# Kernel tuning notes

Measured on AMD Instinct MI355X. Metric: run time of the kernel, lower is better.

## Reference

```python
import jax, jax.numpy as jnp
import numpy as np

N = 50000
E = 800000
D_IN = 384
D_H = 128
D_MLP = 128
K = 16


def layer_norm(x, g, b, eps=1e-5):
    m = x.mean(-1, keepdims=True)
    v = ((x - m) ** 2).mean(-1, keepdims=True)
    return (x - m) / jnp.sqrt(v + eps) * g + b


def setup_inputs() -> dict:
    key = jax.random.key(0)
    ks = jax.random.split(key, 16)
    s = lambda d: 1.0 / np.sqrt(d)
    return {
        "x": jax.random.normal(ks[0], (N, D_IN), jnp.float32),
        "edge_index": jax.random.randint(ks[1], (2, E), 0, N, jnp.int64),
        # GCNConv 1
        "W1": jax.random.normal(ks[2], (D_IN, D_H), jnp.float32) * s(D_IN),
        "b1": jnp.zeros((D_H,), jnp.float32),
        "g1": jnp.ones((D_H,), jnp.float32),
        "be1": jnp.zeros((D_H,), jnp.float32),
        # GCNConv 2
        "W2": jax.random.normal(ks[3], (D_H, D_H), jnp.float32) * s(D_H),
        "b2": jnp.zeros((D_H,), jnp.float32),
        "g2": jnp.ones((D_H,), jnp.float32),
        "be2": jnp.zeros((D_H,), jnp.float32),
        # residual projection (input_dim != conv_hidden)
        "rW": jax.random.normal(ks[4], (D_IN, D_H), jnp.float32) * s(D_IN),
        "rb": jnp.zeros((D_H,), jnp.float32),
        "rg": jnp.ones((D_H,), jnp.float32),
        "rbe": jnp.zeros((D_H,), jnp.float32),
        # MLP head
        "mW1": jax.random.normal(ks[5], (D_H, D_MLP), jnp.float32) * s(D_H),
        "mb1": jnp.zeros((D_MLP,), jnp.float32),
        "mg": jnp.ones((D_MLP,), jnp.float32),
        "mbe": jnp.zeros((D_MLP,), jnp.float32),
        "mW2": jax.random.normal(ks[6], (D_MLP, K), jnp.float32) * s(D_MLP),
        "mb2": jnp.zeros((K,), jnp.float32),
    }


def reference(x, edge_index, W1, b1, g1, be1, W2, b2, g2, be2,
              rW, rb, rg, rbe, mW1, mb1, mg, mbe, mW2, mb2):
    n = x.shape[0]
    loops = jnp.arange(n, dtype=edge_index.dtype)
    src = jnp.concatenate([edge_index[0], loops])  # [E+N]
    dst = jnp.concatenate([edge_index[1], loops])
    # symmetric GCN normalization with self-loops
    deg = jax.ops.segment_sum(jnp.ones_like(src, x.dtype), dst, num_segments=n)
    dinv = jnp.where(deg > 0, jax.lax.rsqrt(deg), 0.0)
    norm = dinv[src] * dinv[dst]  # [E+N]

    def gcn_conv(h, W, b):
        hw = h @ W  # [N, D_H]
        msg = hw[src] * norm[:, None]  # gather + scale, [E+N, D_H]
        return jax.ops.segment_sum(msg, dst, num_segments=n) + b

    # layer 1 with projected residual
    h = jax.nn.elu(layer_norm(gcn_conv(x, W1, b1), g1, be1))
    h = h + layer_norm(x @ rW + rb, rg, rbe)
    # layer 2 with identity residual
    h = jax.nn.elu(layer_norm(gcn_conv(h, W2, b2), g2, be2)) + h
    # MLP head (dropout inactive in eval) + softmax over clusters
    z = jax.nn.elu(layer_norm(h @ mW1 + mb1, mg, mbe))
    H = z @ mW2 + mb2
    return jax.nn.softmax(H, axis=1)
```

## Files before the change

kernel.cpp:

```cpp
#include <hip/hip_runtime.h>

#define DH 128

typedef __attribute__((ext_vector_type(8))) short short8;
typedef __attribute__((ext_vector_type(4))) float f32x4;

__device__ __forceinline__ float wave_sum(float v) {
    #pragma unroll
    for (int o = 32; o > 0; o >>= 1) v += __shfl_xor(v, o, 64);
    return v;
}

__device__ __forceinline__ void ln_pair(float v0, float v1, float& o0, float& o1) {
    float m = wave_sum(v0 + v1) * (1.f / 128.f);
    float d0 = v0 - m, d1 = v1 - m;
    float var = wave_sum(d0 * d0 + d1 * d1) * (1.f / 128.f);
    float inv = rsqrtf(var + 1e-5f);
    o0 = d0 * inv; o1 = d1 * inv;
}

__device__ __forceinline__ float elu(float x) { return x > 0.f ? x : expm1f(x); }

__device__ __forceinline__ unsigned short f2bf(float f) {
    unsigned u = __float_as_uint(f);
    u += 0x7fffu + ((u >> 16) & 1u);
    return (unsigned short)(u >> 16);
}
__device__ __forceinline__ float bfl(unsigned u) { return __uint_as_float(u << 16); }
__device__ __forceinline__ float bfh(unsigned u) { return __uint_as_float(u & 0xffff0000u); }
__device__ __forceinline__ unsigned pack_bf2(float a, float b) {
    return (unsigned)f2bf(a) | ((unsigned)f2bf(b) << 16);
}
__device__ __forceinline__ short8 cvt8(float4 v0, float4 v1) {
    short8 o;
    o[0] = (short)f2bf(v0.x); o[1] = (short)f2bf(v0.y);
    o[2] = (short)f2bf(v0.z); o[3] = (short)f2bf(v0.w);
    o[4] = (short)f2bf(v1.x); o[5] = (short)f2bf(v1.y);
    o[6] = (short)f2bf(v1.z); o[7] = (short)f2bf(v1.w);
    return o;
}

__device__ __forceinline__ int xcd_work(int bid, int nwg) {
    int qc = nwg >> 3, rc = nwg & 7;
    int xcd = bid & 7, ix = bid >> 3;
    return (xcd < rc ? xcd * (qc + 1) : rc * (qc + 1) + (xcd - rc) * qc) + ix;
}

__device__ __forceinline__ void gload_lds16(const unsigned short* gp, unsigned short* lp) {
    __builtin_amdgcn_global_load_lds(
        (const __attribute__((address_space(1))) void*)gp,
        (__attribute__((address_space(3))) void*)lp, 16, 0, 0);
}

__global__ __launch_bounds__(256) void conv_x_k(const float* __restrict__ x,
                                                unsigned short* __restrict__ xb,
                                                long long n8)
{
    long long i = (long long)blockIdx.x * 256 + threadIdx.x;
    long long stride = (long long)gridDim.x * 256;
    for (; i < n8; i += stride) {
        float4 v0 = *(const float4*)(x + i * 8);
        float4 v1 = *(const float4*)(x + i * 8 + 4);
        *(short8*)(xb + i * 8) = cvt8(v0, v1);
    }
}

__global__ void deg_count_k(const int* __restrict__ dst, int* __restrict__ deg, int E) {
    int e = blockIdx.x * 256 + threadIdx.x;
    if (e < E) atomicAdd(&deg[dst[e]], 1);
}

__global__ __launch_bounds__(1024) void scan_part_k(const int* __restrict__ deg,
                                                    int* __restrict__ rowptr,
                                                    int* __restrict__ bsum,
                                                    float* __restrict__ dinv, int n)
{
    __shared__ int wsum[16];
    const int tid = threadIdx.x, lane = tid & 63, wid = tid >> 6;
    int i = blockIdx.x * 1024 + tid;
    int v = (i < n) ? deg[i] : 0;
    if (i < n) dinv[i] = rsqrtf((float)(v + 1));
    int s = v;
    #pragma unroll
    for (int o = 1; o < 64; o <<= 1) {
        int t = __shfl_up(s, o, 64);
        if (lane >= o) s += t;
    }
    if (lane == 63) wsum[wid] = s;
    __syncthreads();
    if (tid < 16) {
        int ws = wsum[tid];
        #pragma unroll
        for (int o = 1; o < 16; o <<= 1) {
            int t = __shfl_up(ws, o, 64);
            if (tid >= o) ws += t;
        }
        wsum[tid] = ws;
    }
    __syncthreads();
    int excl = (wid ? wsum[wid - 1] : 0) + s - v;
    if (i < n) rowptr[i] = excl;
    if (tid == 0) bsum[blockIdx.x] = wsum[15];
}

__global__ void scan_top_k(int* __restrict__ bsum, int* __restrict__ rowptr_n, int nb) {
    int lane = threadIdx.x;
    int carry = 0;
    for (int base = 0; base < nb; base += 64) {
        int i = base + lane;
        int v = (i < nb) ? bsum[i] : 0;
        int s = v;
        #pragma unroll
        for (int o = 1; o < 64; o <<= 1) {
            int t = __shfl_up(s, o, 64);
            if (lane >= o) s += t;
        }
        if (i < nb) bsum[i] = carry + s - v;
        carry += __shfl(s, 63, 64);
    }
    if (lane == 0) *rowptr_n = carry;
}

__global__ void scan_add_k(const int* __restrict__ bsum, int* __restrict__ rowptr,
                           int* __restrict__ cursor, int n)
{
    int i = blockIdx.x * 256 + threadIdx.x;
    if (i < n) {
        int v = rowptr[i] + bsum[i >> 10];
        rowptr[i] = v;
        cursor[i] = v;
    }
}

__global__ __launch_bounds__(256) void fill_xcd_k(
    const int* __restrict__ src, const int* __restrict__ dst,
    const float* __restrict__ dinv, int* __restrict__ cursor,
    int2* __restrict__ csr, int E, int n)
{
    const int g   = blockIdx.x & 7;
    const int j   = blockIdx.x >> 3;
    const int bpg = gridDim.x >> 3;
    const int per = (n + 7) >> 3;
    const int lo = g * per;
    const int hi = min(n, lo + per);
    for (int e = j * 256 + threadIdx.x; e < E; e += bpg * 256) {
        int d = dst[e];
        if (d >= lo && d < hi) {
            int s = src[e];
            float w = dinv[s] * dinv[d];
            int p = atomicAdd(&cursor[d], 1);
            csr[p] = make_int2(s, __float_as_int(w));
        }
    }
}

__global__ void repack_zero_k(const float* __restrict__ W1, const float* __restrict__ rW,
                              const float* __restrict__ W2, const float* __restrict__ mW1,
                              unsigned short* __restrict__ Wp, int* __restrict__ deg, int n)
{
    int idx = blockIdx.x * 256 + threadIdx.x;
    if (idx < n) deg[idx] = 0;
    if (idx >= 131072) return;
    const float* W; int base;
    if (idx < 49152)       { W = W1;  base = 0; }
    else if (idx < 98304)  { W = rW;  base = 49152; }
    else if (idx < 114688) { W = W2;  base = 98304; }
    else                   { W = mW1; base = 114688; }
    int l = idx - base;
    int kb = l >> 12, rem = l & 4095;
    int nn = rem >> 5, ki = rem & 31;
    Wp[idx] = f2bf(W[(kb * 32 + ki) * DH + nn]);
}

__global__ __launch_bounds__(256, 3) void gemm1_k(
    const unsigned short* __restrict__ xb,
    const unsigned short* __restrict__ Bp1, const unsigned short* __restrict__ Bp2,
    const float* __restrict__ bb,
    unsigned short* __restrict__ outa, unsigned short* __restrict__ outb, int n)
{
    constexpr int NT = 6;
    __shared__ __align__(16) unsigned short smem[24576];
    unsigned short* smB = smem + 16384;

    const int tid = threadIdx.x;
    const int wid = tid >> 6, lane = tid & 63;
    const int m16 = lane & 15, q = lane >> 4;

    const int work = xcd_work(blockIdx.x, gridDim.x);
    const int rblk = work >> 2;
    const int var  = work & 3;
    const int mat = var >> 1;
    const int c0  = (var & 1) * 64;
    const unsigned short* Bp = mat ? Bp2 : Bp1;
    unsigned short* outp = mat ? outb : outa;
    const float* bias = mat ? bb : nullptr;
    const long long rowbase = (long long)rblk * 128;

    const unsigned short* gA[4];
    int ldsA[4];
    #pragma unroll
    for (int i = 0; i < 4; ++i) {
        int j = wid * 4 + i;
        int r = j * 8 + (lane >> 3);
        int c = lane & 7;
        long long gr = rowbase + r; if (gr > (long long)n - 1) gr = n - 1;
        gA[i] = xb + gr * 384 + ((c ^ (r & 7)) * 8);
        ldsA[i] = j * 512;
    }
    const unsigned short* gB[2];
    int ldsB[2];
    #pragma unroll
    for (int i = 0; i < 2; ++i) {
        int j2 = wid * 2 + i;
        int cl = j2 * 8 + (lane >> 3);
        int c = lane & 7;
        int cp = c ^ (cl & 7);
        gB[i] = Bp + (cp >> 2) * 4096 + (c0 + cl) * 32 + (cp & 3) * 8;
        ldsB[i] = j2 * 512;
    }

    auto issueT = [&](int t, int buf) {
        #pragma unroll
        for (int i = 0; i < 4; ++i)
            gload_lds16(gA[i] + t * 64, smem + buf * 8192 + ldsA[i]);
        #pragma unroll
        for (int i = 0; i < 2; ++i)
            gload_lds16(gB[i] + t * 8192, smB + buf * 4096 + ldsB[i]);
    };

    f32x4 acc[2][4];
    const f32x4 zero = {0.f, 0.f, 0.f, 0.f};
    #pragma unroll
    for (int mi = 0; mi < 2; ++mi)
        #pragma unroll
        for (int nj = 0; nj < 4; ++nj) acc[mi][nj] = zero;

    const int arow = wid * 32 + m16;
    const int s8a = m16 & 7;

    issueT(0, 0);
    __syncthreads();

    #pragma unroll
    for (int t = 0; t < NT; ++t) {
        const int buf = t & 1;
        if (t + 1 < NT) issueT(t + 1, buf ^ 1);
        const unsigned short* a0 = smem + buf * 8192;
        const unsigned short* b0 = smB + buf * 4096;
        short8 af[2][2], bf[2][4];
        #pragma unroll
        for (int ks = 0; ks < 2; ++ks) {
            int co = ((ks * 4 + q) ^ s8a) * 8;
            af[ks][0] = *(const short8*)(a0 + arow * 64 + co);
            af[ks][1] = *(const short8*)(a0 + (arow + 16) * 64 + co);
            #pragma unroll
            for (int nj = 0; nj < 4; ++nj)
                bf[ks][nj] = *(const short8*)(b0 + (nj * 16 + m16) * 64 + co);
        }
        #pragma unroll
        for (int ks = 0; ks < 2; ++ks)
            #pragma unroll
            for (int nj = 0; nj < 4; ++nj) {
                acc[0][nj] = __builtin_amdgcn_mfma_f32_16x16x32_bf16(af[ks][0], bf[ks][nj], acc[0][nj], 0, 0, 0);
                acc[1][nj] = __builtin_amdgcn_mfma_f32_16x16x32_bf16(af[ks][1], bf[ks][nj], acc[1][nj], 0, 0, 0);
            }
        __syncthreads();
    }

    #pragma unroll
    for (int nj = 0; nj < 4; ++nj) {
        int cl = nj * 16 + m16;
        float bv = bias ? bias[c0 + cl] : 0.f;
        #pragma unroll
        for (int mi = 0; mi < 2; ++mi)
            #pragma unroll
            for (int r = 0; r < 4; ++r)
                smem[(wid * 32 + mi * 16 + q * 4 + r) * 72 + cl] = f2bf(acc[mi][nj][r] + bv);
    }
    __syncthreads();
    #pragma unroll
    for (int h = 0; h < 4; ++h) {
        int idx = tid + h * 256;
        int row = idx >> 3, c8 = idx & 7;
        long long grow = rowbase + row;
        if (grow < n)
            *(short8*)(outp + grow * DH + c0 + c8 * 8) = *(const short8*)(smem + row * 72 + c8 * 8);
    }
}

__global__ __launch_bounds__(256, 3) void gemm_k128(
    const unsigned short* __restrict__ A,
    const unsigned short* __restrict__ Bp, const float* __restrict__ bias,
    unsigned short* __restrict__ outp, int n)
{
    __shared__ __align__(16) unsigned short smem[24576];
    unsigned short* smB = smem + 16384;

    const int tid = threadIdx.x;
    const int wid = tid >> 6, lane = tid & 63;
    const int m16 = lane & 15, q = lane >> 4;

    const int work = xcd_work(blockIdx.x, gridDim.x);
    const int rblk = work >> 1;
    const int c0 = (work & 1) * 64;
    const long long rowbase = (long long)rblk * 128;

    #pragma unroll
    for (int r = 0; r < 8; ++r) {
        int j = r * 256 + tid;
        int row = j >> 4, c16 = j & 15;
        long long grow = rowbase + row; if (grow > (long long)n - 1) grow = n - 1;
        *(short8*)(smem + row * 128 + ((c16 ^ (row & 15)) * 8)) =
            *(const short8*)(A + grow * 128 + c16 * 8);
    }
    #pragma unroll
    for (int r = 0; r < 4; ++r) {
        int j = r * 256 + tid;
        int kb = j >> 8, rem = j & 255;
        int cl = rem >> 2, qq = rem & 3;
        *(short8*)(smB + kb * 2048 + qq * 512 + cl * 8) =
            *(const short8*)(Bp + kb * 4096 + c0 * 32 + rem * 8);
    }
    __syncthreads();

    f32x4 acc[2][4];
    const f32x4 zero = {0.f, 0.f, 0.f, 0.f};
    #pragma unroll
    for (int mi = 0; mi < 2; ++mi)
        #pragma unroll
        for (int nj = 0; nj < 4; ++nj) acc[mi][nj] = zero;

    const int frow = wid * 32 + m16;
    #pragma unroll
    for (int kb = 0; kb < 4; ++kb) {
        short8 af0 = *(const short8*)(smem + frow * 128 + (((kb * 4 + q) ^ m16) * 8));
        short8 af1 = *(const short8*)(smem + (frow + 16) * 128 + (((kb * 4 + q) ^ m16) * 8));
        #pragma unroll
        for (int nj = 0; nj < 4; ++nj) {
            short8 bf = *(const short8*)(smB + kb * 2048 + q * 512 + (nj * 16 + m16) * 8);
            acc[0][nj] = __builtin_amdgcn_mfma_f32_16x16x32_bf16(af0, bf, acc[0][nj], 0, 0, 0);
            acc[1][nj] = __builtin_amdgcn_mfma_f32_16x16x32_bf16(af1, bf, acc[1][nj], 0, 0, 0);
        }
    }

    __syncthreads();
    #pragma unroll
    for (int nj = 0; nj < 4; ++nj) {
        int cl = nj * 16 + m16;
        float bv = bias ? bias[c0 + cl] : 0.f;
        #pragma unroll
        for (int mi = 0; mi < 2; ++mi)
            #pragma unroll
            for (int r = 0; r < 4; ++r)
                smem[(wid * 32 + mi * 16 + q * 4 + r) * 72 + cl] = f2bf(acc[mi][nj][r] + bv);
    }
    __syncthreads();
    #pragma unroll
    for (int h = 0; h < 4; ++h) {
        int idx = tid + h * 256;
        int row = idx >> 3, c8 = idx & 7;
        long long grow = rowbase + row;
        if (grow < n)
            *(short8*)(outp + grow * DH + c0 + c8 * 8) = *(const short8*)(smem + row * 72 + c8 * 8);
    }
}

__device__ __forceinline__ void gather_row(
    const unsigned* __restrict__ hw, const int2* __restrict__ csr,
    int beg, int end, int lane, float& o0, float& o1)
{
    beg = __builtin_amdgcn_readfirstlane(beg);
    end = __builtin_amdgcn_readfirstlane(end);
    float a0 = 0.f, a1 = 0.f, b0 = 0.f, b1 = 0.f;
    float c0 = 0.f, c1 = 0.f, d0 = 0.f, d1 = 0.f;
    int p = beg;
    for (; p + 15 < end; p += 16) {
        int2 e[16];
        #pragma unroll
        for (int i = 0; i < 16; ++i) e[i] = csr[p + i];
        unsigned u[16];
        #pragma unroll
        for (int i = 0; i < 16; ++i) u[i] = hw[(long long)e[i].x * 64 + lane];
        #pragma unroll
        for (int i = 0; i < 16; ++i) {
            float w = __int_as_float(e[i].y);
            float lo = bfl(u[i]), hi = bfh(u[i]);
            if ((i & 3) == 0)      { a0 = fmaf(w, lo, a0); a1 = fmaf(w, hi, a1); }
            else if ((i & 3) == 1) { b0 = fmaf(w, lo, b0); b1 = fmaf(w, hi, b1); }
            else if ((i & 3) == 2) { c0 = fmaf(w, lo, c0); c1 = fmaf(w, hi, c1); }
            else                   { d0 = fmaf(w, lo, d0); d1 = fmaf(w, hi, d1); }
        }
    }
    for (; p + 3 < end; p += 4) {
        int2 e0 = csr[p], e1 = csr[p + 1], e2 = csr[p + 2], e3 = csr[p + 3];
        unsigned u0 = hw[(long long)e0.x * 64 + lane];
        unsigned u1 = hw[(long long)e1.x * 64 + lane];
        unsigned u2 = hw[(long long)e2.x * 64 + lane];
        unsigned u3 = hw[(long long)e3.x * 64 + lane];
        float w0 = __int_as_float(e0.y), w1 = __int_as_float(e1.y);
        float w2 = __int_as_float(e2.y), w3 = __int_as_float(e3.y);
        a0 = fmaf(w0, bfl(u0), a0);  a1 = fmaf(w0, bfh(u0), a1);
        b0 = fmaf(w1, bfl(u1), b0);  b1 = fmaf(w1, bfh(u1), b1);
        c0 = fmaf(w2, bfl(u2), c0);  c1 = fmaf(w2, bfh(u2), c1);
        d0 = fmaf(w3, bfl(u3), d0);  d1 = fmaf(w3, bfh(u3), d1);
    }
    for (; p < end; ++p) {
        int2 e0 = csr[p];
        unsigned u0 = hw[(long long)e0.x * 64 + lane];
        float w0 = __int_as_float(e0.y);
        a0 = fmaf(w0, bfl(u0), a0);
        a1 = fmaf(w0, bfh(u0), a1);
    }
    o0 = (a0 + b0) + (c0 + d0);
    o1 = (a1 + b1) + (c1 + d1);
}

__global__ __launch_bounds__(256) void gfuse1_k(
    const unsigned* __restrict__ hw, const unsigned* __restrict__ proj,
    const int* __restrict__ rowptr, const int2* __restrict__ csr,
    const float* __restrict__ dinv,
    const float* __restrict__ b1, const float* __restrict__ g1, const float* __restrict__ be1,
    const float* __restrict__ rg, const float* __restrict__ rbe,
    unsigned* __restrict__ hout, int n)
{
    int row = blockIdx.x * 4 + (threadIdx.x >> 6);
    if (row >= n) return;
    int lane = threadIdx.x & 63;
    float a0, a1;
    gather_row(hw, csr, rowptr[row], rowptr[row + 1], lane, a0, a1);
    long long off = (long long)row * 64;
    float di = dinv[row], sl = di * di;
    unsigned us = hw[off + lane];
    float2 bv  = *(const float2*)(b1 + 2 * lane);
    float2 gv  = *(const float2*)(g1 + 2 * lane);
    float2 bev = *(const float2*)(be1 + 2 * lane);
    float2 rgv = *(const float2*)(rg + 2 * lane);
    float2 rbv = *(const float2*)(rbe + 2 * lane);
    float v0 = a0 + sl * bfl(us) + bv.x;
    float v1 = a1 + sl * bfh(us) + bv.y;
    float o0, o1; ln_pair(v0, v1, o0, o1);
    float t0 = elu(o0 * gv.x + bev.x);
    float t1 = elu(o1 * gv.y + bev.y);
    unsigned up = proj[off + lane];
    float q0, q1; ln_pair(bfl(up), bfh(up), q0, q1);
    hout[off + lane] = pack_bf2(t0 + q0 * rgv.x + rbv.x, t1 + q1 * rgv.y + rbv.y);
}

__global__ __launch_bounds__(256) void gfuse2_k(
    const unsigned* __restrict__ hw, const unsigned* __restrict__ hprev,
    const int* __restrict__ rowptr, const int2* __restrict__ csr,
    const float* __restrict__ dinv,
    const float* __restrict__ b2, const float* __restrict__ g2, const float* __restrict__ be2,
    unsigned* __restrict__ h2, int n)
{
    int row = blockIdx.x * 4 + (threadIdx.x >> 6);
    if (row >= n) return;
    int lane = threadIdx.x & 63;
    float a0, a1;
    gather_row(hw, csr, rowptr[row], rowptr[row + 1], lane, a0, a1);
    long long off = (long long)row * 64;
    float di = dinv[row], sl = di * di;
    unsigned us = hw[off + lane];
    float2 bv  = *(const float2*)(b2 + 2 * lane);
    float2 gv  = *(const float2*)(g2 + 2 * lane);
    float2 bev = *(const float2*)(be2 + 2 * lane);
    float v0 = a0 + sl * bfl(us) + bv.x;
    float v1 = a1 + sl * bfh(us) + bv.y;
    float o0, o1; ln_pair(v0, v1, o0, o1);
    float t0 = elu(o0 * gv.x + bev.x);
    float t1 = elu(o1 * gv.y + bev.y);
    unsigned uh = hprev[off + lane];
    h2[off + lane] = pack_bf2(t0 + bfl(uh), t1 + bfh(uh));
}

__global__ __launch_bounds__(256) void head_k(
    const unsigned* __restrict__ zraw, const float* __restrict__ g, const float* __restrict__ be,
    const float* __restrict__ mW2, const float* __restrict__ mb2,
    float* __restrict__ out, int n)
{
    int row = blockIdx.x * 4 + (threadIdx.x >> 6);
    if (row >= n) return;
    int lane = threadIdx.x & 63;
    unsigned u = zraw[(long long)row * 64 + lane];
    float o0, o1; ln_pair(bfl(u), bfh(u), o0, o1);
    float2 gv  = *(const float2*)(g + 2 * lane);
    float2 bev = *(const float2*)(be + 2 * lane);
    float z0 = elu(o0 * gv.x + bev.x);
    float z1 = elu(o1 * gv.y + bev.y);
    int k = lane & 15, seg = lane >> 4;
    float acc = 0.f;
    #pragma unroll
    for (int t = 0; t < 16; ++t) {
        int srcl = seg * 16 + t;
        float zz0 = __shfl(z0, srcl, 64);
        float zz1 = __shfl(z1, srcl, 64);
        int c = seg * 32 + 2 * t;
        acc = fmaf(zz0, mW2[c * 16 + k], acc);
        acc = fmaf(zz1, mW2[(c + 1) * 16 + k], acc);
    }
    acc += __shfl_xor(acc, 32, 64);
    acc += __shfl_xor(acc, 16, 64);
    float hk = acc + mb2[k];
    float mx = hk;
    #pragma unroll
    for (int o = 8; o > 0; o >>= 1) mx = fmaxf(mx, __shfl_xor(mx, o, 64));
    float e = expf(hk - mx);
    float s = e;
    #pragma unroll
    for (int o = 8; o > 0; o >>= 1) s += __shfl_xor(s, o, 64);
    if (lane < 16) out[(long long)row * 16 + k] = e / s;
}

static inline size_t align16(size_t x) { return (x + 15) & ~(size_t)15; }

extern "C" void kernel_launch(void* const* d_in, const int* in_sizes, int n_in,
                              void* d_out, int out_size, void* d_ws, size_t ws_size,
                              hipStream_t stream)
{
    const float* x   = (const float*)d_in[0];
    const int*   ei  = (const int*)d_in[1];
    const float* W1  = (const float*)d_in[2];
    const float* b1  = (const float*)d_in[3];
    const float* g1  = (const float*)d_in[4];
    const float* be1 = (const float*)d_in[5];
    const float* W2  = (const float*)d_in[6];
    const float* b2  = (const float*)d_in[7];
    const float* g2  = (const float*)d_in[8];
    const float* be2 = (const float*)d_in[9];
    const float* rW  = (const float*)d_in[10];
    const float* rb  = (const float*)d_in[11];
    const float* rg  = (const float*)d_in[12];
    const float* rbe = (const float*)d_in[13];
    const float* mW1 = (const float*)d_in[14];
    const float* mb1 = (const float*)d_in[15];
    const float* mg  = (const float*)d_in[16];
    const float* mbe = (const float*)d_in[17];
    const float* mW2 = (const float*)d_in[18];
    const float* mb2 = (const float*)d_in[19];
    float* out = (float*)d_out;

    const int n = in_sizes[0] / 384;
    const int E = in_sizes[1] / 2;
    const int* src = ei;
    const int* dst = ei + E;

    char* w = (char*)d_ws;
    int* deg     = (int*)w;   w += align16((size_t)n * 4);
    int* rowptr  = (int*)w;   w += align16((size_t)(n + 1) * 4);
    int* cursor  = (int*)w;   w += align16((size_t)n * 4);
    float* dinv  = (float*)w; w += align16((size_t)n * 4);
    int* bsum    = (int*)w;   w += align16((size_t)1024 * 4);
    int2* csr    = (int2*)w;  w += align16((size_t)E * 8);
    unsigned short* xb   = (unsigned short*)w; w += align16((size_t)n * 384 * 2);
    unsigned short* hw1  = (unsigned short*)w; w += align16((size_t)n * DH * 2);
    unsigned short* proj = (unsigned short*)w; w += align16((size_t)n * DH * 2);
    unsigned short* hbuf = (unsigned short*)w; w += align16((size_t)n * DH * 2);
    unsigned short* Wp   = (unsigned short*)w; w += align16((size_t)131072 * 2);
    unsigned short* Wp1 = Wp;
    unsigned short* Wpr = Wp + 49152;
    unsigned short* Wp2 = Wp + 98304;
    unsigned short* WpM = Wp + 114688;
    unsigned short* hw2  = hw1;
    unsigned short* h2   = proj;
    unsigned short* zraw = hbuf;

    int gE = (E + 255) / 256;
    int gN = (n + 255) / 256;
    int nb = (n + 1023) / 1024;
    int rblks = (n + 127) / 128;
    int gRow4 = (n + 3) / 4;

    conv_x_k<<<2048, 256, 0, stream>>>(x, xb, (long long)n * 48);
    repack_zero_k<<<512, 256, 0, stream>>>(W1, rW, W2, mW1, Wp, deg, n);

    deg_count_k<<<gE, 256, 0, stream>>>(dst, deg, E);
    scan_part_k<<<nb, 1024, 0, stream>>>(deg, rowptr, bsum, dinv, n);
    scan_top_k<<<1, 64, 0, stream>>>(bsum, rowptr + n, nb);
    scan_add_k<<<gN, 256, 0, stream>>>(bsum, rowptr, cursor, n);
    fill_xcd_k<<<1024, 256, 0, stream>>>(src, dst, dinv, cursor, csr, E, n);

    gemm1_k<<<rblks * 4, 256, 0, stream>>>(xb, Wp1, Wpr, rb, hw1, proj, n);
    gfuse1_k<<<gRow4, 256, 0, stream>>>((unsigned*)hw1, (unsigned*)proj, rowptr, csr, dinv,
                                        b1, g1, be1, rg, rbe, (unsigned*)hbuf, n);

    gemm_k128<<<rblks * 2, 256, 0, stream>>>(hbuf, Wp2, nullptr, hw2, n);
    gfuse2_k<<<gRow4, 256, 0, stream>>>((unsigned*)hw2, (unsigned*)hbuf, rowptr, csr, dinv,
                                        b2, g2, be2, (unsigned*)h2, n);

    gemm_k128<<<rblks * 2, 256, 0, stream>>>(h2, WpM, mb1, zraw, n);
    head_k<<<gRow4, 256, 0, stream>>>((unsigned*)zraw, mg, mbe, mW2, mb2, out, n);
}
```

Before: 402.3 us.

## Fuse fp32-to-bf16 input conversion into first GEMM by loading fp32 tiles to LDS

```diff
diff --git a/kernel.cpp b/kernel.cpp
--- a/kernel.cpp
+++ b/kernel.cpp
@@ -46,23 +46,10 @@
     return (xcd < rc ? xcd * (qc + 1) : rc * (qc + 1) + (xcd - rc) * qc) + ix;
 }
 
-__device__ __forceinline__ void gload_lds16(const unsigned short* gp, unsigned short* lp) {
+__device__ __forceinline__ void gload_lds16(const void* gp, void* lp) {
     __builtin_amdgcn_global_load_lds(
         (const __attribute__((address_space(1))) void*)gp,
         (__attribute__((address_space(3))) void*)lp, 16, 0, 0);
-}
-
-__global__ __launch_bounds__(256) void conv_x_k(const float* __restrict__ x,
-                                                unsigned short* __restrict__ xb,
-                                                long long n8)
-{
-    long long i = (long long)blockIdx.x * 256 + threadIdx.x;
-    long long stride = (long long)gridDim.x * 256;
-    for (; i < n8; i += stride) {
-        float4 v0 = *(const float4*)(x + i * 8);
-        float4 v1 = *(const float4*)(x + i * 8 + 4);
-        *(short8*)(xb + i * 8) = cvt8(v0, v1);
-    }
 }
 
 __global__ void deg_count_k(const int* __restrict__ dst, int* __restrict__ deg, int E) {
@@ -172,15 +159,16 @@
     Wp[idx] = f2bf(W[(kb * 32 + ki) * DH + nn]);
 }
 
-__global__ __launch_bounds__(256, 3) void gemm1_k(
-    const unsigned short* __restrict__ xb,
+__global__ __launch_bounds__(256, 2) void gemm1_k(
+    const float* __restrict__ x,
     const unsigned short* __restrict__ Bp1, const unsigned short* __restrict__ Bp2,
     const float* __restrict__ bb,
     unsigned short* __restrict__ outa, unsigned short* __restrict__ outb, int n)
 {
     constexpr int NT = 6;
-    __shared__ __align__(16) unsigned short smem[24576];
-    unsigned short* smB = smem + 16384;
+    __shared__ __align__(16) unsigned char smraw[81920];
+    float* smA = (float*)smraw;
+    unsigned short* smB = (unsigned short*)(smraw + 65536);
 
     const int tid = threadIdx.x;
     const int wid = tid >> 6, lane = tid & 63;
@@ -196,16 +184,16 @@
     const float* bias = mat ? bb : nullptr;
     const long long rowbase = (long long)rblk * 128;
 
-    const unsigned short* gA[4];
-    int ldsA[4];
-    #pragma unroll
-    for (int i = 0; i < 4; ++i) {
-        int j = wid * 4 + i;
-        int r = j * 8 + (lane >> 3);
-        int c = lane & 7;
+    const float* gA[8];
+    int ldsA[8];
+    #pragma unroll
+    for (int i = 0; i < 8; ++i) {
+        int j = wid * 8 + i;
+        int r = j * 4 + (lane >> 4);
+        int c = lane & 15;
         long long gr = rowbase + r; if (gr > (long long)n - 1) gr = n - 1;
-        gA[i] = xb + gr * 384 + ((c ^ (r & 7)) * 8);
-        ldsA[i] = j * 512;
+        gA[i] = x + gr * 384 + ((c ^ (r & 15)) * 4);
+        ldsA[i] = j * 256;
     }
     const unsigned short* gB[2];
     int ldsB[2];
@@ -221,8 +209,8 @@
 
     auto issueT = [&](int t, int buf) {
         #pragma unroll
-        for (int i = 0; i < 4; ++i)
-            gload_lds16(gA[i] + t * 64, smem + buf * 8192 + ldsA[i]);
+        for (int i = 0; i < 8; ++i)
+            gload_lds16(gA[i] + t * 64, smA + buf * 8192 + ldsA[i]);
         #pragma unroll
         for (int i = 0; i < 2; ++i)
             gload_lds16(gB[i] + t * 8192, smB + buf * 4096 + ldsB[i]);
@@ -236,7 +224,7 @@
         for (int nj = 0; nj < 4; ++nj) acc[mi][nj] = zero;
 
     const int arow = wid * 32 + m16;
-    const int s8a = m16 & 7;
+    const int s8b = m16 & 7;
 
     issueT(0, 0);
     __syncthreads();
@@ -245,14 +233,23 @@
     for (int t = 0; t < NT; ++t) {
         const int buf = t & 1;
         if (t + 1 < NT) issueT(t + 1, buf ^ 1);
-        const unsigned short* a0 = smem + buf * 8192;
+        const float* a0 = smA + buf * 8192;
         const unsigned short* b0 = smB + buf * 4096;
         short8 af[2][2], bf[2][4];
         #pragma unroll
         for (int ks = 0; ks < 2; ++ks) {
-            int co = ((ks * 4 + q) ^ s8a) * 8;
-            af[ks][0] = *(const short8*)(a0 + arow * 64 + co);
-            af[ks][1] = *(const short8*)(a0 + (arow + 16) * 64 + co);
+            int g0 = ks * 8 + q * 2;
+            {
+                float4 lo = *(const float4*)(a0 + arow * 64 + ((g0 ^ m16) * 4));
+                float4 hi = *(const float4*)(a0 + arow * 64 + (((g0 + 1) ^ m16) * 4));
+                af[ks][0] = cvt8(lo, hi);
+            }
+            {
+                float4 lo = *(const float4*)(a0 + (arow + 16) * 64 + ((g0 ^ m16) * 4));
+                float4 hi = *(const float4*)(a0 + (arow + 16) * 64 + (((g0 + 1) ^ m16) * 4));
+                af[ks][1] = cvt8(lo, hi);
+            }
+            int co = ((ks * 4 + q) ^ s8b) * 8;
             #pragma unroll
             for (int nj = 0; nj < 4; ++nj)
                 bf[ks][nj] = *(const short8*)(b0 + (nj * 16 + m16) * 64 + co);
@@ -267,6 +264,7 @@
         __syncthreads();
     }
 
+    unsigned short* ep = (unsigned short*)smraw;
     #pragma unroll
     for (int nj = 0; nj < 4; ++nj) {
         int cl = nj * 16 + m16;
@@ -275,7 +273,7 @@
         for (int mi = 0; mi < 2; ++mi)
             #pragma unroll
             for (int r = 0; r < 4; ++r)
-                smem[(wid * 32 + mi * 16 + q * 4 + r) * 72 + cl] = f2bf(acc[mi][nj][r] + bv);
+                ep[(wid * 32 + mi * 16 + q * 4 + r) * 72 + cl] = f2bf(acc[mi][nj][r] + bv);
     }
     __syncthreads();
     #pragma unroll
@@ -284,7 +282,7 @@
         int row = idx >> 3, c8 = idx & 7;
         long long grow = rowbase + row;
         if (grow < n)
-            *(short8*)(outp + grow * DH + c0 + c8 * 8) = *(const short8*)(smem + row * 72 + c8 * 8);
+            *(short8*)(outp + grow * DH + c0 + c8 * 8) = *(const short8*)(ep + row * 72 + c8 * 8);
     }
 }
 
@@ -551,7 +549,6 @@
     float* dinv  = (float*)w; w += align16((size_t)n * 4);
     int* bsum    = (int*)w;   w += align16((size_t)1024 * 4);
     int2* csr    = (int2*)w;  w += align16((size_t)E * 8);
-    unsigned short* xb   = (unsigned short*)w; w += align16((size_t)n * 384 * 2);
     unsigned short* hw1  = (unsigned short*)w; w += align16((size_t)n * DH * 2);
     unsigned short* proj = (unsigned short*)w; w += align16((size_t)n * DH * 2);
     unsigned short* hbuf = (unsigned short*)w; w += align16((size_t)n * DH * 2);
@@ -570,7 +567,6 @@
     int rblks = (n + 127) / 128;
     int gRow4 = (n + 3) / 4;
 
-    conv_x_k<<<2048, 256, 0, stream>>>(x, xb, (long long)n * 48);
     repack_zero_k<<<512, 256, 0, stream>>>(W1, rW, W2, mW1, Wp, deg, n);
 
     deg_count_k<<<gE, 256, 0, stream>>>(dst, deg, E);
@@ -579,7 +575,7 @@
     scan_add_k<<<gN, 256, 0, stream>>>(bsum, rowptr, cursor, n);
     fill_xcd_k<<<1024, 256, 0, stream>>>(src, dst, dinv, cursor, csr, E, n);
 
-    gemm1_k<<<rblks * 4, 256, 0, stream>>>(xb, Wp1, Wpr, rb, hw1, proj, n);
+    gemm1_k<<<rblks * 4, 256, 0, stream>>>(x, Wp1, Wpr, rb, hw1, proj, n);
     gfuse1_k<<<gRow4, 256, 0, stream>>>((unsigned*)hw1, (unsigned*)proj, rowptr, csr, dinv,
                                         b1, g1, be1, rg, rbe, (unsigned*)hbuf, n);
 
```

Result: no change. 408.1 us (+1.4%).
